# Optimization experiments

Measured on AMD Instinct MI355X. Metric: run time of the kernel, lower is better.

The kernel has to match this reference:

```python
import jax, jax.numpy as jnp
import numpy as np

EPS = 1e-5
NUM_HEADS = 12
PATCH = 16

def layernorm(x, g, b):
    m = jnp.mean(x, axis=-1, keepdims=True)
    v = jnp.var(x, axis=-1, keepdims=True)
    return (x - m) / jnp.sqrt(v + EPS) * g + b

def setup_inputs() -> dict:
    key = jax.random.key(0)
    ks = jax.random.split(key, 10)
    B, C, H, D, L = 32, 3, 224, 768, 12
    Dff, NCLS = 3072, 5
    N = (H // PATCH) ** 2 + 1  # 197 tokens incl. cls
    def rn(k, shape, s=0.02):
        return jax.random.normal(k, shape, jnp.float32) * s
    return {
        "x": jax.random.normal(ks[0], (B, C, H, H), jnp.float32),
        "conv_w": rn(ks[1], (D, C, PATCH, PATCH)),
        "conv_b": jnp.zeros((D,), jnp.float32),
        "cls_token": rn(ks[2], (1, 1, D)),
        "pos_embed": rn(ks[3], (1, N, D)),
        "ln1_g": jnp.ones((L, D), jnp.float32), "ln1_b": jnp.zeros((L, D), jnp.float32),
        "qkv_w": rn(ks[4], (L, D, 3 * D)), "qkv_b": jnp.zeros((L, 3 * D), jnp.float32),
        "proj_w": rn(ks[5], (L, D, D)), "proj_b": jnp.zeros((L, D), jnp.float32),
        "ln2_g": jnp.ones((L, D), jnp.float32), "ln2_b": jnp.zeros((L, D), jnp.float32),
        "fc1_w": rn(ks[6], (L, D, Dff)), "fc1_b": jnp.zeros((L, Dff), jnp.float32),
        "fc2_w": rn(ks[7], (L, Dff, D)), "fc2_b": jnp.zeros((L, D), jnp.float32),
        "norm_g": jnp.ones((D,), jnp.float32), "norm_b": jnp.zeros((D,), jnp.float32),
        "head_w": rn(ks[8], (D, NCLS)), "head_b": jnp.zeros((NCLS,), jnp.float32),
    }

def reference(x, conv_w, conv_b, cls_token, pos_embed,
              ln1_g, ln1_b, qkv_w, qkv_b, proj_w, proj_b,
              ln2_g, ln2_b, fc1_w, fc1_b, fc2_w, fc2_b,
              norm_g, norm_b, head_w, head_b):
    B = x.shape[0]
    D = conv_w.shape[0]
    HD = D // NUM_HEADS
    scale = HD ** -0.5
    # patch embedding: conv stride=kernel=16 -> [B, D, 14, 14]
    p = jax.lax.conv_general_dilated(
        x, conv_w, (PATCH, PATCH), 'VALID',
        dimension_numbers=('NCHW', 'OIHW', 'NCHW')) + conv_b[None, :, None, None]
    tok = p.reshape(B, D, -1).transpose(0, 2, 1)  # [B, Np, D]
    tok = jnp.concatenate([jnp.broadcast_to(cls_token, (B, 1, D)), tok], axis=1)
    tok = tok + pos_embed  # [B, N, D]; dropout is identity at eval

    def block(h, params):
        l1g, l1b, qw, qb, pw, pb, l2g, l2b, f1w, f1b, f2w, f2b = params
        y = layernorm(h, l1g, l1b)
        qkv = (y @ qw + qb).reshape(B, -1, 3, NUM_HEADS, HD)
        q, k, v = qkv[:, :, 0], qkv[:, :, 1], qkv[:, :, 2]  # [B, N, H, HD]
        attn = jax.nn.softmax(jnp.einsum('bqhd,bkhd->bhqk', q, k) * scale, axis=-1)
        o = jnp.einsum('bhqk,bkhd->bqhd', attn, v).reshape(B, -1, D)
        h = h + (o @ pw + pb)
        y = layernorm(h, l2g, l2b)
        h = h + (jax.nn.gelu(y @ f1w + f1b, approximate=False) @ f2w + f2b)
        return h, None

    tok, _ = jax.lax.scan(
        block, tok,
        (ln1_g, ln1_b, qkv_w, qkv_b, proj_w, proj_b,
         ln2_g, ln2_b, fc1_w, fc1_b, fc2_w, fc2_b))
    cls = layernorm(tok, norm_g, norm_b)[:, 0]  # [B, D]
    return cls @ head_w + head_b  # [B, num_classes]
```

## Files before the change

kernel.cpp:

```cpp
#include <hip/hip_runtime.h>
#include <hip/hip_bf16.h>
#include <math.h>

#define B_      32
#define NTOK    197
#define NPATCH  196
#define D_      768
#define DFF     3072
#define L_      12
#define NH      12
#define HD      64
#define NCLS    5
#define MTOK    (B_ * NTOK)
#define MPAD    6400
#define MPATCH  (B_ * NPATCH)
#define KPAD    224
#define KS_STR  72
#define VT_STR  232

typedef __attribute__((ext_vector_type(8))) short short8;
typedef __attribute__((ext_vector_type(4))) float floatx4;

static __device__ inline short f2bf(float f) {
  __hip_bfloat16 h = __float2bfloat16(f);
  short s; __builtin_memcpy(&s, &h, 2); return s;
}

__global__ __launch_bounds__(256) void cls_pos_kernel(
    const float* __restrict__ cls, const float* __restrict__ pos,
    float* __restrict__ tok) {
  int i = blockIdx.x * 256 + threadIdx.x;
  if (i < B_ * D_) {
    int b = i / D_, d = i % D_;
    tok[(size_t)b * NTOK * D_ + d] = cls[d] + pos[d];
  }
}

__global__ __launch_bounds__(256) void cvt_kernel(
    const float* __restrict__ src, short* __restrict__ dst, int n) {
  int i = blockIdx.x * 256 + threadIdx.x;
  if (i < n) dst[i] = f2bf(src[i]);
}

__global__ __launch_bounds__(256) void wconv_all_kernel(
    const float* __restrict__ qw, const float* __restrict__ pw,
    const float* __restrict__ f1w, const float* __restrict__ f2w,
    short* __restrict__ wq, short* __restrict__ wp,
    short* __restrict__ w1, short* __restrict__ w2) {
  int id = blockIdx.x;
  const float* W; short* Wt; int K, N, t;
  if (id < 1728)      { W = qw;  Wt = wq; K = 768;  N = 2304; t = id; }
  else if (id < 2304) { W = pw;  Wt = wp; K = 768;  N = 768;  t = id - 1728; }
  else if (id < 4608) { W = f1w; Wt = w1; K = 768;  N = 3072; t = id - 2304; }
  else                { W = f2w; Wt = w2; K = 3072; N = 768;  t = id - 4608; }
  int ntn = N >> 5;
  int k0 = (t / ntn) * 32, n0 = (t % ntn) * 32;
  __shared__ float tt[32][33];
  int tid = threadIdx.x;
#pragma unroll
  for (int q = 0; q < 4; q++) {
    int e = q * 256 + tid;
    int rk = e >> 5, cn = e & 31;
    tt[rk][cn] = W[(size_t)(k0 + rk) * N + n0 + cn];
  }
  __syncthreads();
#pragma unroll
  for (int q = 0; q < 4; q++) {
    int e = q * 256 + tid;
    int rn = e >> 5, ck = e & 31;
    Wt[(size_t)(n0 + rn) * K + k0 + ck] = f2bf(tt[ck][rn]);
  }
}

__global__ __launch_bounds__(256) void im2col_kernel(
    const float* __restrict__ x, short* __restrict__ Abf) {
  int i = blockIdx.x * 256 + threadIdx.x;
  if (i >= MPATCH * D_) return;
  int row = i / D_, col = i % D_;
  int b = row / NPATCH, n = row % NPATCH;
  int ph = n / 14, pw = n % 14;
  int c = col >> 8, r = col & 255;
  int kh = r >> 4, kw = r & 15;
  Abf[i] = f2bf(x[(((size_t)b * 3 + c) * 224 + (ph * 16 + kh)) * 224 + (pw * 16 + kw)]);
}

__global__ __launch_bounds__(256) void patch_scatter_kernel(
    const float* __restrict__ po, const float* __restrict__ pos,
    float* __restrict__ tok) {
  int i = blockIdx.x * 256 + threadIdx.x;
  if (i >= MPATCH * D_) return;
  int row = i / D_, col = i % D_;
  int b = row / NPATCH, n = row % NPATCH;
  tok[((size_t)b * NTOK + 1 + n) * D_ + col] = po[i] + pos[(size_t)(1 + n) * D_ + col];
}

template <bool OBF>
__global__ __launch_bounds__(256) void ln_kernel(
    const float* __restrict__ in, void* __restrict__ out,
    const float* __restrict__ g, const float* __restrict__ bt,
    long rs_in) {
  int row = blockIdx.x;
  const float* xr = in + (size_t)row * rs_in;
  int tid = threadIdx.x;
  float v0 = xr[tid], v1 = xr[tid + 256], v2 = xr[tid + 512];
  float s = v0 + v1 + v2;
#pragma unroll
  for (int off = 32; off; off >>= 1) s += __shfl_xor(s, off);
  __shared__ float red1[4], red2[4];
  int wid = tid >> 6, lane = tid & 63;
  if (lane == 0) red1[wid] = s;
  __syncthreads();
  float mean = (red1[0] + red1[1] + red1[2] + red1[3]) * (1.f / 768.f);
  float d0 = v0 - mean, d1 = v1 - mean, d2 = v2 - mean;
  float s2 = d0 * d0 + d1 * d1 + d2 * d2;
#pragma unroll
  for (int off = 32; off; off >>= 1) s2 += __shfl_xor(s2, off);
  if (lane == 0) red2[wid] = s2;
  __syncthreads();
  float var = (red2[0] + red2[1] + red2[2] + red2[3]) * (1.f / 768.f);
  float rstd = rsqrtf(var + 1e-5f);
  float o0 = d0 * rstd * g[tid]       + bt[tid];
  float o1 = d1 * rstd * g[tid + 256] + bt[tid + 256];
  float o2 = d2 * rstd * g[tid + 512] + bt[tid + 512];
  if (OBF) {
    short* yr = (short*)out + (size_t)row * D_;
    yr[tid] = f2bf(o0); yr[tid + 256] = f2bf(o1); yr[tid + 512] = f2bf(o2);
  } else {
    float* yr = (float*)out + (size_t)row * D_;
    yr[tid] = o0; yr[tid + 256] = o1; yr[tid + 512] = o2;
  }
}

template <int BM, bool OBF, bool RES, bool GELU_>
__global__ __launch_bounds__(256) void gemm_db_kernel(
    const short* __restrict__ A, const short* __restrict__ Wt,
    const float* __restrict__ bias, const float* __restrict__ res,
    void* __restrict__ Cout, int M, int N, int K) {
  constexpr int NBI = (BM == 128) ? 2 : 4;
  __shared__ short As[2][BM * 32];
  __shared__ short Bs[2][128 * 32];
  const int tid = threadIdx.x;
  const int lane = tid & 63;
  const int wid = tid >> 6;
  const int wave_m = (BM == 128) ? (wid >> 1) : 0;
  const int wave_n = (BM == 128) ? (wid & 1) : wid;
  const int mbase = blockIdx.y * BM;
  const int nbase = blockIdx.x * 128;

  const int lrow = lane >> 2;
  const int kbg = (lane & 3) ^ ((lane >> 3) & 3);

  const short* gA0 = A + (size_t)(mbase + wid * 32 + lrow) * K + kbg * 8;
  const short* gA1 = gA0 + 16 * (size_t)K;
  const int brow0 = (BM == 128) ? (wid * 32) : (wid * 64);
  const short* gB[NBI];
  gB[0] = Wt + (size_t)(nbase + brow0 + lrow) * K + kbg * 8;
#pragma unroll
  for (int c = 1; c < NBI; c++) gB[c] = gB[0] + (size_t)c * 16 * K;

  typedef const __attribute__((address_space(1))) unsigned* gp_t;
  typedef __attribute__((address_space(3))) unsigned* lp_t;
  const int aoff = wid * 1024;
  const int boff = brow0 * 32;

  __builtin_amdgcn_global_load_lds((gp_t)(const void*)gA0, (lp_t)(void*)(&As[0][aoff]), 16, 0, 0);
  __builtin_amdgcn_global_load_lds((gp_t)(const void*)gA1, (lp_t)(void*)(&As[0][aoff + 512]), 16, 0, 0);
#pragma unroll
  for (int c = 0; c < NBI; c++)
    __builtin_amdgcn_global_load_lds((gp_t)(const void*)gB[c], (lp_t)(void*)(&Bs[0][boff + c * 512]), 16, 0, 0);

  floatx4 zero = {0.f, 0.f, 0.f, 0.f};
  floatx4 acc[4][4];
#pragma unroll
  for (int i = 0; i < 4; i++)
#pragma unroll
    for (int j = 0; j < 4; j++) acc[i][j] = zero;

  const int quad = lane >> 4;
  const int l15 = lane & 15;
  const int s = quad ^ ((l15 >> 1) & 3);

  const int niter = K >> 5;
  for (int it = 0; it < niter; it++) {
    const int cur = it & 1, nxt = cur ^ 1;
    __syncthreads();
    if (it + 1 < niter) {
      const int ks = (it + 1) << 5;
      __builtin_amdgcn_global_load_lds((gp_t)(const void*)(gA0 + ks), (lp_t)(void*)(&As[nxt][aoff]), 16, 0, 0);
      __builtin_amdgcn_global_load_lds((gp_t)(const void*)(gA1 + ks), (lp_t)(void*)(&As[nxt][aoff + 512]), 16, 0, 0);
#pragma unroll
      for (int c = 0; c < NBI; c++)
        __builtin_amdgcn_global_load_lds((gp_t)(const void*)(gB[c] + ks), (lp_t)(void*)(&Bs[nxt][boff + c * 512]), 16, 0, 0);
    }
    short8 a[4], b[4];
#pragma unroll
    for (int i = 0; i < 4; i++) {
      a[i] = *(const short8*)(&As[cur][(wave_m * 64 + i * 16 + l15) * 32 + s * 8]);
      b[i] = *(const short8*)(&Bs[cur][(wave_n * 64 + i * 16 + l15) * 32 + s * 8]);
    }
#pragma unroll
    for (int i = 0; i < 4; i++)
#pragma unroll
      for (int j = 0; j < 4; j++)
        acc[i][j] = __builtin_amdgcn_mfma_f32_16x16x32_bf16(a[i], b[j], acc[i][j], 0, 0, 0);
  }

#pragma unroll
  for (int i = 0; i < 4; i++) {
    int gm0 = mbase + wave_m * 64 + i * 16 + quad * 4;
#pragma unroll
    for (int r = 0; r < 4; r++) {
      int gm = gm0 + r;
      if (gm >= M) continue;
#pragma unroll
      for (int j = 0; j < 4; j++) {
        int gn = nbase + wave_n * 64 + j * 16 + l15;
        float c = acc[i][j][r] + bias[gn];
        if (RES) c += res[(size_t)gm * N + gn];
        if (GELU_) c = 0.5f * c * (1.f + erff(c * 0.70710678118654752f));
        if (OBF) ((short*)Cout)[(size_t)gm * N + gn] = f2bf(c);
        else ((float*)Cout)[(size_t)gm * N + gn] = c;
      }
    }
  }
}

__global__ __launch_bounds__(256) void attn_mfma_kernel(
    const short* __restrict__ qkv, short* __restrict__ o) {
  __shared__ short Ks[KPAD * KS_STR];
  __shared__ short Vt[64 * VT_STR];
  __shared__ short Pw[4 * 16 * VT_STR];
  const int h = blockIdx.x % NH;
  const int b = blockIdx.x / NH;
  const int tid = threadIdx.x;
  const int lane = tid & 63, wid = tid >> 6;
  const size_t rowbase = (size_t)b * NTOK * (3 * D_);

  for (int it = 0; it < 7; it++) {
    int idx = it * 256 + tid;
    int dblk = idx / KPAD, key = idx % KPAD;
    int krow = key < NTOK ? key : NTOK - 1;
    const short* src = qkv + rowbase + (size_t)krow * (3 * D_) + h * HD;
    short8 kv = *(const short8*)(src + D_ + dblk * 8);
    *(short8*)(Ks + key * KS_STR + dblk * 8) = kv;
    short8 vv = *(const short8*)(src + 2 * D_ + dblk * 8);
#pragma unroll
    for (int i = 0; i < 8; i++) Vt[(dblk * 8 + i) * VT_STR + key] = vv[i];
  }
  __syncthreads();

  const int quad = lane >> 4, l15 = lane & 15;
  short* P = Pw + wid * 16 * VT_STR;
  const floatx4 zero = {0.f, 0.f, 0.f, 0.f};

  for (int qt = wid; qt < 14; qt += 4) {
    int qrow = qt * 16 + l15;
    int qr = qrow < NTOK ? qrow : NTOK - 1;
    const short* qbase = qkv + rowbase + (size_t)qr * (3 * D_) + h * HD;
    short8 a0 = *(const short8*)(qbase + quad * 8);
    short8 a1 = *(const short8*)(qbase + 32 + quad * 8);

    floatx4 s[14];
#pragma unroll
    for (int kt = 0; kt < 14; kt++) {
      const short* kb = Ks + (kt * 16 + l15) * KS_STR;
      short8 b0 = *(const short8*)(kb + quad * 8);
      short8 b1 = *(const short8*)(kb + 32 + quad * 8);
      floatx4 c = __builtin_amdgcn_mfma_f32_16x16x32_bf16(a0, b0, zero, 0, 0, 0);
      s[kt] = __builtin_amdgcn_mfma_f32_16x16x32_bf16(a1, b1, c, 0, 0, 0);
    }
#pragma unroll
    for (int kt = 0; kt < 14; kt++) {
      if (kt * 16 + l15 >= NTOK) {
#pragma unroll
        for (int r = 0; r < 4; r++) s[kt][r] = -1e30f;
      }
    }
    float mx[4] = {-1e30f, -1e30f, -1e30f, -1e30f};
#pragma unroll
    for (int kt = 0; kt < 14; kt++)
#pragma unroll
      for (int r = 0; r < 4; r++) mx[r] = fmaxf(mx[r], s[kt][r]);
#pragma unroll
    for (int off = 1; off < 16; off <<= 1)
#pragma unroll
      for (int r = 0; r < 4; r++) mx[r] = fmaxf(mx[r], __shfl_xor(mx[r], off));
    float lsum[4] = {0.f, 0.f, 0.f, 0.f};
#pragma unroll
    for (int kt = 0; kt < 14; kt++) {
#pragma unroll
      for (int r = 0; r < 4; r++) {
        float p = __expf(0.125f * (s[kt][r] - mx[r]));
        lsum[r] += p;
        P[(quad * 4 + r) * VT_STR + kt * 16 + l15] = f2bf(p);
      }
    }
#pragma unroll
    for (int off = 1; off < 16; off <<= 1)
#pragma unroll
      for (int r = 0; r < 4; r++) lsum[r] += __shfl_xor(lsum[r], off);
    float inv[4];
#pragma unroll
    for (int r = 0; r < 4; r++) inv[r] = 1.f / lsum[r];

    floatx4 oacc[4] = {zero, zero, zero, zero};
#pragma unroll
    for (int kk = 0; kk < 7; kk++) {
      short8 a = *(const short8*)(P + l15 * VT_STR + kk * 32 + quad * 8);
#pragma unroll
      for (int nt = 0; nt < 4; nt++) {
        short8 bv = *(const short8*)(Vt + (nt * 16 + l15) * VT_STR + kk * 32 + quad * 8);
        oacc[nt] = __builtin_amdgcn_mfma_f32_16x16x32_bf16(a, bv, oacc[nt], 0, 0, 0);
      }
    }
#pragma unroll
    for (int r = 0; r < 4; r++) {
      int q = qt * 16 + quad * 4 + r;
      if (q >= NTOK) continue;
      short* orow = o + ((size_t)(b * NTOK + q)) * D_ + h * HD;
#pragma unroll
      for (int nt = 0; nt < 4; nt++)
        orow[nt * 16 + l15] = f2bf(oacc[nt][r] * inv[r]);
    }
  }
}

__global__ __launch_bounds__(64) void head_kernel(
    const float* __restrict__ y, const float* __restrict__ hw,
    const float* __restrict__ hb, float* __restrict__ out) {
  int b = blockIdx.x;
  const float* yr = y + (size_t)b * D_;
  int lane = threadIdx.x;
  for (int j = 0; j < NCLS; j++) {
    float s = 0.f;
    for (int d = lane; d < D_; d += 64) s += yr[d] * hw[(size_t)d * NCLS + j];
#pragma unroll
    for (int off = 32; off; off >>= 1) s += __shfl_xor(s, off);
    if (lane == 0) out[b * NCLS + j] = s + hb[j];
  }
}

extern "C" void kernel_launch(void* const* d_in, const int* in_sizes, int n_in,
                              void* d_out, int out_size, void* d_ws, size_t ws_size,
                              hipStream_t stream) {
  const float* x        = (const float*)d_in[0];
  const float* conv_w   = (const float*)d_in[1];
  const float* conv_b   = (const float*)d_in[2];
  const float* cls_tok  = (const float*)d_in[3];
  const float* pos_emb  = (const float*)d_in[4];
  const float* ln1_g    = (const float*)d_in[5];
  const float* ln1_b    = (const float*)d_in[6];
  const float* qkv_w    = (const float*)d_in[7];
  const float* qkv_b    = (const float*)d_in[8];
  const float* proj_w   = (const float*)d_in[9];
  const float* proj_b   = (const float*)d_in[10];
  const float* ln2_g    = (const float*)d_in[11];
  const float* ln2_b    = (const float*)d_in[12];
  const float* fc1_w    = (const float*)d_in[13];
  const float* fc1_b    = (const float*)d_in[14];
  const float* fc2_w    = (const float*)d_in[15];
  const float* fc2_b    = (const float*)d_in[16];
  const float* norm_g   = (const float*)d_in[17];
  const float* norm_b   = (const float*)d_in[18];
  const float* head_w   = (const float*)d_in[19];
  const float* head_b   = (const float*)d_in[20];
  float* out = (float*)d_out;

  char* p = (char*)d_ws;
  float* tok    = (float*)p;                 p += (size_t)MTOK * D_ * 4;
  short* y_bf   = (short*)p;                 p += (size_t)MPAD * D_ * 2;
  short* o_bf   = (short*)p;                 p += (size_t)MPAD * D_ * 2;
  short* h_bf   = (short*)p;                 p += (size_t)MPAD * DFF * 2;
  short* wt_qkv = (short*)p;                 p += (size_t)D_ * 3 * D_ * 2;
  short* wt_prj = (short*)p;                 p += (size_t)D_ * D_ * 2;
  short* wt_fc1 = (short*)p;                 p += (size_t)D_ * DFF * 2;
  short* wt_fc2 = (short*)p;                 p += (size_t)DFF * D_ * 2;
  short* cw_bf  = (short*)p;                 p += (size_t)D_ * D_ * 2;
  short* im_bf  = (short*)p;                 p += (size_t)MPAD * D_ * 2;
  float* big1   = (float*)p;                 p += (size_t)MTOK * 3 * D_ * 4;
  short* qkv_bf = (short*)big1;
  float* pout   = big1;
  float* yf     = (float*)(p);

  cvt_kernel<<<(D_ * D_ + 255) / 256, 256, 0, stream>>>(conv_w, cw_bf, D_ * D_);
  im2col_kernel<<<(MPATCH * D_ + 255) / 256, 256, 0, stream>>>(x, im_bf);
  cls_pos_kernel<<<(B_ * D_ + 255) / 256, 256, 0, stream>>>(cls_tok, pos_emb, tok);
  {
    dim3 g(D_ / 128, MPATCH / 64);
    gemm_db_kernel<64, false, false, false><<<g, 128, 0, stream>>>(
        im_bf, cw_bf, conv_b, nullptr, pout, MPATCH, D_, D_);
  }
  patch_scatter_kernel<<<(MPATCH * D_ + 255) / 256, 256, 0, stream>>>(pout, pos_emb, tok);

  dim3 gQKV(3 * D_ / 128, (MTOK + 127) / 128);
  dim3 gPRJ(D_ / 128, (MTOK + 63) / 64);
  dim3 gFC1(DFF / 128, (MTOK + 127) / 128);
  dim3 gFC2(D_ / 128, (MTOK + 63) / 64);

  for (int l = 0; l < L_; l++) {
    const float* l1g = ln1_g + l * D_;
    const float* l1b = ln1_b + l * D_;
    const float* qw  = qkv_w + (size_t)l * D_ * 3 * D_;
    const float* qb  = qkv_b + (size_t)l * 3 * D_;
    const float* pw  = proj_w + (size_t)l * D_ * D_;
    const float* pb  = proj_b + (size_t)l * D_;
    const float* l2g = ln2_g + l * D_;
    const float* l2b = ln2_b + l * D_;
    const float* f1w = fc1_w + (size_t)l * D_ * DFF;
    const float* f1b = fc1_b + (size_t)l * DFF;
    const float* f2w = fc2_w + (size_t)l * DFF * D_;
    const float* f2b = fc2_b + (size_t)l * D_;

    wconv_all_kernel<<<6912, 256, 0, stream>>>(qw, pw, f1w, f2w,
                                               wt_qkv, wt_prj, wt_fc1, wt_fc2);

    ln_kernel<true><<<MTOK, 256, 0, stream>>>(tok, y_bf, l1g, l1b, D_);
    gemm_db_kernel<128, true, false, false><<<gQKV, 256, 0, stream>>>(
        y_bf, wt_qkv, qb, nullptr, qkv_bf, MTOK, 3 * D_, D_);
    attn_mfma_kernel<<<B_ * NH, 256, 0, stream>>>(qkv_bf, o_bf);
    gemm_db_kernel<64, false, true, false><<<gPRJ, 128, 0, stream>>>(
        o_bf, wt_prj, pb, tok, tok, MTOK, D_, D_);
    ln_kernel<true><<<MTOK, 256, 0, stream>>>(tok, y_bf, l2g, l2b, D_);
    gemm_db_kernel<128, true, false, true><<<gFC1, 256, 0, stream>>>(
        y_bf, wt_fc1, f1b, nullptr, h_bf, MTOK, DFF, D_);
    gemm_db_kernel<64, false, true, false><<<gFC2, 128, 0, stream>>>(
        h_bf, wt_fc2, f2b, tok, tok, MTOK, D_, DFF);
  }

  ln_kernel<false><<<B_, 256, 0, stream>>>(tok, yf, norm_g, norm_b, (long)NTOK * D_);
  head_kernel<<<B_, 64, 0, stream>>>(yf, head_w, head_b, out);
}
```

Measured before the change: 3.689 ms.

## Split-K the FC2 GEMM into three slices with a separate reduce kernel

The FC2 GEMM (K=3072) now runs with BM=128 tiles and a grid z-dimension of 3. Each slice covers 1024 of K and writes fp32 partial sums into a scratch buffer. A new reduce kernel then adds the three partials, the bias and the residual into the token buffer. The aim is better parallelism and shorter per-block K loops than the 64-row, 128-thread version, at the cost of extra fp32 partial traffic (three M×N buffers written and read) and one more launch per layer.

```diff
diff --git a/kernel.cpp b/kernel.cpp
--- a/kernel.cpp
+++ b/kernel.cpp
@@ -131,11 +131,11 @@
   }
 }
 
-template <int BM, bool OBF, bool RES, bool GELU_>
+template <int BM, bool OBF, bool RES, bool GELU_, bool SPLITK = false>
 __global__ __launch_bounds__(256) void gemm_db_kernel(
     const short* __restrict__ A, const short* __restrict__ Wt,
     const float* __restrict__ bias, const float* __restrict__ res,
-    void* __restrict__ Cout, int M, int N, int K) {
+    void* __restrict__ Cout, int M, int N, int K, int kslice) {
   constexpr int NBI = (BM == 128) ? 2 : 4;
   __shared__ short As[2][BM * 32];
   __shared__ short Bs[2][128 * 32];
@@ -146,15 +146,16 @@
   const int wave_n = (BM == 128) ? (wid & 1) : wid;
   const int mbase = blockIdx.y * BM;
   const int nbase = blockIdx.x * 128;
+  const int kbase = SPLITK ? blockIdx.z * kslice : 0;
 
   const int lrow = lane >> 2;
   const int kbg = (lane & 3) ^ ((lane >> 3) & 3);
 
-  const short* gA0 = A + (size_t)(mbase + wid * 32 + lrow) * K + kbg * 8;
+  const short* gA0 = A + (size_t)(mbase + wid * 32 + lrow) * K + kbase + kbg * 8;
   const short* gA1 = gA0 + 16 * (size_t)K;
   const int brow0 = (BM == 128) ? (wid * 32) : (wid * 64);
   const short* gB[NBI];
-  gB[0] = Wt + (size_t)(nbase + brow0 + lrow) * K + kbg * 8;
+  gB[0] = Wt + (size_t)(nbase + brow0 + lrow) * K + kbase + kbg * 8;
 #pragma unroll
   for (int c = 1; c < NBI; c++) gB[c] = gB[0] + (size_t)c * 16 * K;
 
@@ -180,7 +181,7 @@
   const int l15 = lane & 15;
   const int s = quad ^ ((l15 >> 1) & 3);
 
-  const int niter = K >> 5;
+  const int niter = kslice >> 5;
   for (int it = 0; it < niter; it++) {
     const int cur = it & 1, nxt = cur ^ 1;
     __syncthreads();
@@ -215,14 +216,35 @@
 #pragma unroll
       for (int j = 0; j < 4; j++) {
         int gn = nbase + wave_n * 64 + j * 16 + l15;
-        float c = acc[i][j][r] + bias[gn];
-        if (RES) c += res[(size_t)gm * N + gn];
-        if (GELU_) c = 0.5f * c * (1.f + erff(c * 0.70710678118654752f));
-        if (OBF) ((short*)Cout)[(size_t)gm * N + gn] = f2bf(c);
-        else ((float*)Cout)[(size_t)gm * N + gn] = c;
+        if constexpr (SPLITK) {
+          ((float*)Cout)[(size_t)blockIdx.z * M * N + (size_t)gm * N + gn] = acc[i][j][r];
+        } else {
+          float c = acc[i][j][r] + bias[gn];
+          if (RES) c += res[(size_t)gm * N + gn];
+          if (GELU_) c = 0.5f * c * (1.f + erff(c * 0.70710678118654752f));
+          if (OBF) ((short*)Cout)[(size_t)gm * N + gn] = f2bf(c);
+          else ((float*)Cout)[(size_t)gm * N + gn] = c;
+        }
       }
     }
   }
+}
+
+__global__ __launch_bounds__(256) void fc2_reduce_kernel(
+    const float* __restrict__ part, const float* __restrict__ bias,
+    float* __restrict__ tok) {
+  const size_t MN = (size_t)MTOK * D_;
+  size_t i = ((size_t)blockIdx.x * 256 + threadIdx.x) * 4;
+  if (i >= MN) return;
+  floatx4 p0 = *(const floatx4*)(part + i);
+  floatx4 p1 = *(const floatx4*)(part + i + MN);
+  floatx4 p2 = *(const floatx4*)(part + i + 2 * MN);
+  floatx4 t  = *(const floatx4*)(tok + i);
+  int col = (int)(i % D_);
+  floatx4 o;
+#pragma unroll
+  for (int r = 0; r < 4; r++) o[r] = t[r] + bias[col + r] + p0[r] + p1[r] + p2[r];
+  *(floatx4*)(tok + i) = o;
 }
 
 __global__ __launch_bounds__(256) void attn_mfma_kernel(
@@ -380,6 +402,7 @@
   float* big1   = (float*)p;                 p += (size_t)MTOK * 3 * D_ * 4;
   short* qkv_bf = (short*)big1;
   float* pout   = big1;
+  float* fc2_part = big1;
   float* yf     = (float*)(p);
 
   cvt_kernel<<<(D_ * D_ + 255) / 256, 256, 0, stream>>>(conv_w, cw_bf, D_ * D_);
@@ -388,14 +411,14 @@
   {
     dim3 g(D_ / 128, MPATCH / 64);
     gemm_db_kernel<64, false, false, false><<<g, 128, 0, stream>>>(
-        im_bf, cw_bf, conv_b, nullptr, pout, MPATCH, D_, D_);
+        im_bf, cw_bf, conv_b, nullptr, pout, MPATCH, D_, D_, D_);
   }
   patch_scatter_kernel<<<(MPATCH * D_ + 255) / 256, 256, 0, stream>>>(pout, pos_emb, tok);
 
   dim3 gQKV(3 * D_ / 128, (MTOK + 127) / 128);
   dim3 gPRJ(D_ / 128, (MTOK + 63) / 64);
   dim3 gFC1(DFF / 128, (MTOK + 127) / 128);
-  dim3 gFC2(D_ / 128, (MTOK + 63) / 64);
+  dim3 gFC2(D_ / 128, (MTOK + 127) / 128, 3);
 
   for (int l = 0; l < L_; l++) {
     const float* l1g = ln1_g + l * D_;
@@ -416,15 +439,17 @@
 
     ln_kernel<true><<<MTOK, 256, 0, stream>>>(tok, y_bf, l1g, l1b, D_);
     gemm_db_kernel<128, true, false, false><<<gQKV, 256, 0, stream>>>(
-        y_bf, wt_qkv, qb, nullptr, qkv_bf, MTOK, 3 * D_, D_);
+        y_bf, wt_qkv, qb, nullptr, qkv_bf, MTOK, 3 * D_, D_, D_);
     attn_mfma_kernel<<<B_ * NH, 256, 0, stream>>>(qkv_bf, o_bf);
     gemm_db_kernel<64, false, true, false><<<gPRJ, 128, 0, stream>>>(
-        o_bf, wt_prj, pb, tok, tok, MTOK, D_, D_);
+        o_bf, wt_prj, pb, tok, tok, MTOK, D_, D_, D_);
     ln_kernel<true><<<MTOK, 256, 0, stream>>>(tok, y_bf, l2g, l2b, D_);
     gemm_db_kernel<128, true, false, true><<<gFC1, 256, 0, stream>>>(
-        y_bf, wt_fc1, f1b, nullptr, h_bf, MTOK, DFF, D_);
-    gemm_db_kernel<64, false, true, false><<<gFC2, 128, 0, stream>>>(
-        h_bf, wt_fc2, f2b, tok, tok, MTOK, D_, DFF);
+        y_bf, wt_fc1, f1b, nullptr, h_bf, MTOK, DFF, D_, D_);
+    gemm_db_kernel<128, false, false, false, true><<<gFC2, 256, 0, stream>>>(
+        h_bf, wt_fc2, nullptr, nullptr, fc2_part, MTOK, D_, DFF, 1024);
+    fc2_reduce_kernel<<<(MTOK * D_ / 4 + 255) / 256, 256, 0, stream>>>(
+        fc2_part, f2b, tok);
   }
 
   ln_kernel<false><<<B_, 256, 0, stream>>>(tok, yf, norm_g, norm_b, (long)NTOK * D_);
```

Result: faster. 3.549 ms (-3.8%).
